# Kernel tuning notes

Measured on AMD Instinct MI355X. Metric: run time of the kernel, lower is better.

The kernel has to match this reference:

```python
import jax, jax.numpy as jnp
import numpy as np
from jax import lax

B, N = 2, 8192
H = W = 256
KNN_K = 33          # includes self, as in _computeDensity
RADIUS = 0.1
CUTOFF = 1.0        # cutOffThreshold: a dx^2 + b dy^2 + c dx dy <= cutoffC
WIN = 9             # fixed splat footprint (ellipse extents ~1-3 px, clamped at 15 in source)
EPS = 1e-8


def setup_inputs() -> dict:
    key = jax.random.key(0)
    k1, k2, k3, k4, k5 = jax.random.split(key, 5)
    points = jax.random.normal(k1, (B, N, 3), jnp.float32)
    # projected pixel coordinates, kept a few px inside the image
    proj_xy = jax.random.uniform(k2, (B, N, 2), jnp.float32, 4.0, W - 4.0)
    # ellipse coefficients a, b, c with 4ab - c^2 > 0 (valid ellipse)
    ab = jax.random.uniform(k3, (B, N, 2), jnp.float32, 0.1, 0.5)
    c = jax.random.uniform(k4, (B, N, 1), jnp.float32, -0.05, 0.05)
    ellipse_params = jnp.concatenate([ab, c], axis=-1)
    colors = jax.random.uniform(k5, (B, N, 3), jnp.float32)
    return {"points": points, "proj_xy": proj_xy,
            "ellipse_params": ellipse_params, "colors": colors}


def _compute_density(points):
    # faithful jax version of _computeDensity: KNN gaussian density
    r2 = RADIUS * RADIUS
    sq = jnp.sum(points * points, axis=-1)                      # [B,N]
    # pairwise squared distances [B,N,N]
    d2 = sq[:, :, None] + sq[:, None, :] - 2.0 * jnp.einsum('bnd,bmd->bnm', points, points)
    neg_d2k, _ = lax.top_k(-d2, KNN_K)                          # k nearest (incl. self)
    d2k = jnp.maximum(-neg_d2k[:, :, 1:], 0.0)                  # drop self, [B,N,K-1]
    w = jnp.exp(-d2k / r2 / 4.0)
    w = jnp.where(d2k > r2, 0.0, w)
    return jnp.sum(w, axis=-1)                                  # [B,N]


def reference(points, proj_xy, ellipse_params, colors):
    density = _compute_density(points)                          # [B,N]
    a = ellipse_params[..., 0]
    b = ellipse_params[..., 1]
    c = ellipse_params[..., 2]
    x = proj_xy[..., 0]
    y = proj_xy[..., 1]
    # _findEllipseBoundingBox extents, clamped at 15 as in the grad path
    den = 4.0 * a * b - c * c
    xE = jnp.minimum(jnp.sqrt(4.0 * b * CUTOFF / den), 15.0)    # [B,N]
    yE = jnp.minimum(jnp.sqrt(4.0 * a * CUTOFF / den), 15.0)

    # fixed WINxWIN footprint around floor(proj) (jit-friendly bbox)
    R = WIN // 2
    offs = jnp.arange(-R, R + 1, dtype=jnp.float32)
    ox, oy = jnp.meshgrid(offs, offs, indexing='ij')
    ox = ox.reshape(-1)                                         # [P]
    oy = oy.reshape(-1)
    x0 = jnp.floor(x)
    y0 = jnp.floor(y)
    px = x0[..., None] + ox                                     # [B,N,P]
    py = y0[..., None] + oy
    dx = px - x[..., None]
    dy = py - y[..., None]
    # elliptical gaussian splat weight, truncated at cutoff
    Q = a[..., None] * dx * dx + b[..., None] * dy * dy + c[..., None] * dx * dy
    inb = (px >= 0) & (px < W) & (py >= 0) & (py < H)
    bbox = (jnp.abs(dx) <= xE[..., None] + 1.0) & (jnp.abs(dy) <= yE[..., None] + 1.0)
    mask = inb & bbox & (Q <= CUTOFF)
    w = jnp.where(mask, jnp.exp(-0.5 * Q) * density[..., None], 0.0)  # [B,N,P]

    # scatter-accumulate weighted colors and weights per pixel
    pxi = jnp.clip(px.astype(jnp.int32), 0, W - 1)
    pyi = jnp.clip(py.astype(jnp.int32), 0, H - 1)
    bi = jnp.arange(B, dtype=jnp.int32)[:, None, None]
    flat = ((bi * H + pyi) * W + pxi).reshape(-1)               # [B*N*P]
    wc = (w[..., None] * colors[:, :, None, :]).reshape(-1, 3)
    wf = w.reshape(-1)
    img_c = jnp.zeros((B * H * W, 3), jnp.float32).at[flat].add(wc)
    img_w = jnp.zeros((B * H * W,), jnp.float32).at[flat].add(wf)
    image = img_c / (img_w[:, None] + EPS)
    return image.reshape(B, H, W, 3)
```

## Files before the change

kernel.cpp:

```cpp
#include <hip/hip_runtime.h>

#define NB  2
#define NP  8192
#define IMH 256
#define IMW 256
#define NBKT 1024
#define CAP 128

constexpr float R2F = 0.01f;
constexpr float BK_SCALE = 64.f;
constexpr float BK_OFF   = 8.f;
#define BK_PAD 7

__device__ __forceinline__ int bucket_of(float x) {
    int b = (int)floorf((x + BK_OFF) * BK_SCALE);
    return min(max(b, 0), NBKT - 1);
}

__device__ __forceinline__ float sq_np(float x, float y, float z) {
    return __fadd_rn(__fadd_rn(__fmul_rn(x, x), __fmul_rn(y, y)),
                     __fmul_rn(z, z));
}

__global__ __launch_bounds__(256) void init_kernel(
    float4* __restrict__ out4, float4* __restrict__ imgw4, int4* __restrict__ cnt4)
{
    const int t = blockIdx.x * 256 + threadIdx.x;
    const float4 z4 = make_float4(0.f, 0.f, 0.f, 0.f);
    if (t < 98304)       out4[t] = z4;
    else if (t < 131072) imgw4[t - 98304] = z4;
    if (t < 512)         cnt4[t] = make_int4(0, 0, 0, 0);
}

__global__ __launch_bounds__(256) void binfill_kernel(
    const float* __restrict__ pts, float4* __restrict__ bins,
    int* __restrict__ counts)
{
    const int t = blockIdx.x * 256 + threadIdx.x;
    const int b = t >> 13, i = t & (NP - 1);
    const float x = pts[(size_t)t * 3 + 0];
    const float y = pts[(size_t)t * 3 + 1];
    const float z = pts[(size_t)t * 3 + 2];
    const int g = (b << 10) + bucket_of(x);
    const int slot = atomicAdd(&counts[g], 1);
    if (slot < CAP)
        bins[(size_t)g * CAP + slot] = make_float4(x, y, z, __int_as_float(i));
}

__global__ __launch_bounds__(1024) void densplat_kernel(
    const float4* __restrict__ bins, const int* __restrict__ counts,
    const float* __restrict__ proj, const float* __restrict__ ell,
    const float* __restrict__ cols,
    float* __restrict__ img_c, float* __restrict__ img_w)
{
    const int bk = blockIdx.x;
    const int b  = bk >> 10, kb = bk & (NBKT - 1);
    const int wave = threadIdx.x >> 6, lane = threadIdx.x & 63;
    const int cnt = min(counts[bk], CAP);
    const int s0  = wave * 8;
    if (s0 >= cnt) return;
    const int nv = min(8, cnt - s0);

    float xi[8], yi[8], zi[8], sqi[8], sum[8];
    int   oi[8];
    #pragma unroll
    for (int u = 0; u < 8; ++u) {
        const int si = s0 + min(u, nv - 1);
        const float4 p = bins[(size_t)bk * CAP + si];
        xi[u] = p.x; yi[u] = p.y; zi[u] = p.z;
        sqi[u] = sq_np(p.x, p.y, p.z);
        oi[u] = __float_as_int(p.w);
        sum[u] = 0.f;
    }

    const int jb0 = max(kb - BK_PAD, 0), jb1 = min(kb + BK_PAD, NBKT - 1);
    for (int jb = jb0; jb <= jb1; ++jb) {
        const int gj = (b << 10) + jb;
        const int cj = min(counts[gj], CAP);
        const float4* __restrict__ bp = bins + (size_t)gj * CAP;
        const bool own = (jb == kb);
        for (int jj = lane; jj < cj; jj += 64) {
            const float4 pj = bp[jj];
            const float sqj = sq_np(pj.x, pj.y, pj.z);
            #pragma unroll
            for (int u = 0; u < 8; ++u) {
                const float dot = __fmaf_rn(zi[u], pj.z,
                                  __fmaf_rn(yi[u], pj.y,
                                  __fmul_rn(xi[u], pj.x)));
                const float d2 = __fsub_rn(__fadd_rn(sqi[u], sqj),
                                           __fadd_rn(dot, dot));
                const float d2c = fmaxf(d2, 0.f);
                if (!(own && jj == s0 + u) && d2c <= R2F)
                    sum[u] += expf(__fmul_rn(__fdiv_rn(d2c, R2F), -0.25f));
            }
        }
    }

    for (int u = 0; u < nv; ++u) {
        float s = sum[u];
        #pragma unroll
        for (int off2 = 32; off2; off2 >>= 1) s += __shfl_down(s, off2, 64);
        const float dens = __shfl(s, 0, 64);
        if (dens == 0.f) continue;

        const size_t gp = (size_t)b * NP + oi[u];
        const float x = proj[gp * 2 + 0], y = proj[gp * 2 + 1];
        const float a  = ell[gp * 3 + 0], bb = ell[gp * 3 + 1], c = ell[gp * 3 + 2];
        const float cr = cols[gp * 3 + 0], cg = cols[gp * 3 + 1], cb = cols[gp * 3 + 2];

        const float den = __fsub_rn(__fmul_rn(__fmul_rn(4.f, a), bb),
                                    __fmul_rn(c, c));
        const float xE = fminf(__fsqrt_rn(__fdiv_rn(__fmul_rn(4.f, bb), den)), 15.f);
        const float yE = fminf(__fsqrt_rn(__fdiv_rn(__fmul_rn(4.f, a),  den)), 15.f);
        const float xEp1 = __fadd_rn(xE, 1.f);
        const float yEp1 = __fadd_rn(yE, 1.f);
        const float x0 = floorf(x), y0 = floorf(y);

        for (int idx = lane; idx < 81; idx += 64) {
            const float ox = (float)(idx / 9) - 4.f;
            const float oy = (float)(idx % 9) - 4.f;
            const float px = __fadd_rn(x0, ox);
            const float py = __fadd_rn(y0, oy);
            if (px < 0.f || px >= 256.f || py < 0.f || py >= 256.f) continue;
            const float dx = __fsub_rn(px, x);
            const float dy = __fsub_rn(py, y);
            if (fabsf(dx) > xEp1 || fabsf(dy) > yEp1) continue;
            const float Q = __fadd_rn(__fadd_rn(
                                __fmul_rn(__fmul_rn(a, dx), dx),
                                __fmul_rn(__fmul_rn(bb, dy), dy)),
                              __fmul_rn(__fmul_rn(c, dx), dy));
            if (!(Q <= 1.0f)) continue;
            const float wgt = __fmul_rn(expf(__fmul_rn(-0.5f, Q)), dens);
            const int pxi = (int)px, pyi = (int)py;
            const int flat = ((b << 8) + pyi) * IMW + pxi;
            atomicAdd(&img_c[flat * 3 + 0], __fmul_rn(wgt, cr));
            atomicAdd(&img_c[flat * 3 + 1], __fmul_rn(wgt, cg));
            atomicAdd(&img_c[flat * 3 + 2], __fmul_rn(wgt, cb));
            atomicAdd(&img_w[flat],         wgt);
        }
    }
}

__global__ __launch_bounds__(256) void norm_kernel(
    float* __restrict__ out, const float* __restrict__ img_w)
{
    const int p = blockIdx.x * 256 + threadIdx.x;
    if (p < NB * IMH * IMW) {
        const float d = __fadd_rn(img_w[p], 1e-8f);
        out[3 * p + 0] = __fdiv_rn(out[3 * p + 0], d);
        out[3 * p + 1] = __fdiv_rn(out[3 * p + 1], d);
        out[3 * p + 2] = __fdiv_rn(out[3 * p + 2], d);
    }
}

extern "C" void kernel_launch(void* const* d_in, const int* in_sizes, int n_in,
                              void* d_out, int out_size, void* d_ws, size_t ws_size,
                              hipStream_t stream)
{
    const float* points = (const float*)d_in[0];
    const float* proj   = (const float*)d_in[1];
    const float* ell    = (const float*)d_in[2];
    const float* cols   = (const float*)d_in[3];
    float* out = (float*)d_out;

    float4* bins   = (float4*)d_ws;
    float*  img_w  = (float*)(bins + (size_t)NB * NBKT * CAP);
    int*    counts = (int*)(img_w + (size_t)NB * IMH * IMW);

    init_kernel    <<<512, 256, 0, stream>>>((float4*)out, (float4*)img_w,
                                             (int4*)counts);
    binfill_kernel <<<NB * NP / 256, 256, 0, stream>>>(points, bins, counts);
    densplat_kernel<<<NB * NBKT, 1024, 0, stream>>>(bins, counts,
                                                    proj, ell, cols, out, img_w);
    norm_kernel    <<<(NB * IMH * IMW + 255) / 256, 256, 0, stream>>>(out, img_w);
}
```

Before: 49.84 us.

## Map one wave per bucket looping over its points, zero buffers with memset

Each bucket used to get a 1024-thread block where each wave handled 8 points. Now each wave owns a whole bucket and loops over its points in groups of 8, with four buckets per 256-thread block. Neighbor bucket counts and pointers are loaded once per wave. The aim is to cut the many mostly idle waves and block launches, since buckets average about 8 points. The image accumulators move to workspace, and the init kernel is replaced by a single hipMemsetAsync over image and count buffers, so norm now reads from img_c. The trade-off is less parallelism for crowded buckets, which are now processed serially within one wave.

```diff
diff --git a/kernel.cpp b/kernel.cpp
--- a/kernel.cpp
+++ b/kernel.cpp
@@ -22,16 +22,6 @@
                      __fmul_rn(z, z));
 }
 
-__global__ __launch_bounds__(256) void init_kernel(
-    float4* __restrict__ out4, float4* __restrict__ imgw4, int4* __restrict__ cnt4)
-{
-    const int t = blockIdx.x * 256 + threadIdx.x;
-    const float4 z4 = make_float4(0.f, 0.f, 0.f, 0.f);
-    if (t < 98304)       out4[t] = z4;
-    else if (t < 131072) imgw4[t - 98304] = z4;
-    if (t < 512)         cnt4[t] = make_int4(0, 0, 0, 0);
-}
-
 __global__ __launch_bounds__(256) void binfill_kernel(
     const float* __restrict__ pts, float4* __restrict__ bins,
     int* __restrict__ counts)
@@ -47,109 +37,120 @@
         bins[(size_t)g * CAP + slot] = make_float4(x, y, z, __int_as_float(i));
 }
 
-__global__ __launch_bounds__(1024) void densplat_kernel(
+__global__ __launch_bounds__(256) void densplat_kernel(
     const float4* __restrict__ bins, const int* __restrict__ counts,
     const float* __restrict__ proj, const float* __restrict__ ell,
     const float* __restrict__ cols,
     float* __restrict__ img_c, float* __restrict__ img_w)
 {
-    const int bk = blockIdx.x;
+    const int wave = threadIdx.x >> 6, lane = threadIdx.x & 63;
+    const int bk = blockIdx.x * 4 + wave;
     const int b  = bk >> 10, kb = bk & (NBKT - 1);
-    const int wave = threadIdx.x >> 6, lane = threadIdx.x & 63;
     const int cnt = min(counts[bk], CAP);
-    const int s0  = wave * 8;
-    if (s0 >= cnt) return;
-    const int nv = min(8, cnt - s0);
-
-    float xi[8], yi[8], zi[8], sqi[8], sum[8];
-    int   oi[8];
-    #pragma unroll
-    for (int u = 0; u < 8; ++u) {
-        const int si = s0 + min(u, nv - 1);
-        const float4 p = bins[(size_t)bk * CAP + si];
-        xi[u] = p.x; yi[u] = p.y; zi[u] = p.z;
-        sqi[u] = sq_np(p.x, p.y, p.z);
-        oi[u] = __float_as_int(p.w);
-        sum[u] = 0.f;
-    }
+    if (cnt == 0) return;
 
     const int jb0 = max(kb - BK_PAD, 0), jb1 = min(kb + BK_PAD, NBKT - 1);
-    for (int jb = jb0; jb <= jb1; ++jb) {
-        const int gj = (b << 10) + jb;
-        const int cj = min(counts[gj], CAP);
-        const float4* __restrict__ bp = bins + (size_t)gj * CAP;
-        const bool own = (jb == kb);
-        for (int jj = lane; jj < cj; jj += 64) {
-            const float4 pj = bp[jj];
-            const float sqj = sq_np(pj.x, pj.y, pj.z);
-            #pragma unroll
-            for (int u = 0; u < 8; ++u) {
-                const float dot = __fmaf_rn(zi[u], pj.z,
-                                  __fmaf_rn(yi[u], pj.y,
-                                  __fmul_rn(xi[u], pj.x)));
-                const float d2 = __fsub_rn(__fadd_rn(sqi[u], sqj),
-                                           __fadd_rn(dot, dot));
-                const float d2c = fmaxf(d2, 0.f);
-                if (!(own && jj == s0 + u) && d2c <= R2F)
-                    sum[u] += expf(__fmul_rn(__fdiv_rn(d2c, R2F), -0.25f));
+    int cj[15]; const float4* bp[15];
+    const int nw = jb1 - jb0 + 1;
+    for (int m = 0; m < nw; ++m) {
+        const int gj = (b << 10) + (jb0 + m);
+        cj[m] = min(counts[gj], CAP);
+        bp[m] = bins + (size_t)gj * CAP;
+    }
+    const int ownm = kb - jb0;
+
+    for (int s0 = 0; s0 < cnt; s0 += 8) {
+        const int nv = min(8, cnt - s0);
+
+        float xi[8], yi[8], zi[8], sqi[8], sum[8];
+        int   oi[8];
+        #pragma unroll
+        for (int u = 0; u < 8; ++u) {
+            const int si = s0 + min(u, nv - 1);
+            const float4 p = bins[(size_t)bk * CAP + si];
+            xi[u] = p.x; yi[u] = p.y; zi[u] = p.z;
+            sqi[u] = sq_np(p.x, p.y, p.z);
+            oi[u] = __float_as_int(p.w);
+            sum[u] = 0.f;
+        }
+
+        for (int m = 0; m < nw; ++m) {
+            const bool own = (m == ownm);
+            const float4* __restrict__ bj = bp[m];
+            const int c = cj[m];
+            for (int jj = lane; jj < c; jj += 64) {
+                const float4 pj = bj[jj];
+                const float sqj = sq_np(pj.x, pj.y, pj.z);
+                #pragma unroll
+                for (int u = 0; u < 8; ++u) {
+                    const float dot = __fmaf_rn(zi[u], pj.z,
+                                      __fmaf_rn(yi[u], pj.y,
+                                      __fmul_rn(xi[u], pj.x)));
+                    const float d2 = __fsub_rn(__fadd_rn(sqi[u], sqj),
+                                               __fadd_rn(dot, dot));
+                    const float d2c = fmaxf(d2, 0.f);
+                    if (!(own && jj == s0 + u) && d2c <= R2F)
+                        sum[u] += expf(__fmul_rn(__fdiv_rn(d2c, R2F), -0.25f));
+                }
             }
         }
-    }
 
-    for (int u = 0; u < nv; ++u) {
-        float s = sum[u];
-        #pragma unroll
-        for (int off2 = 32; off2; off2 >>= 1) s += __shfl_down(s, off2, 64);
-        const float dens = __shfl(s, 0, 64);
-        if (dens == 0.f) continue;
+        for (int u = 0; u < nv; ++u) {
+            float s = sum[u];
+            #pragma unroll
+            for (int off2 = 32; off2; off2 >>= 1) s += __shfl_down(s, off2, 64);
+            const float dens = __shfl(s, 0, 64);
+            if (dens == 0.f) continue;
 
-        const size_t gp = (size_t)b * NP + oi[u];
-        const float x = proj[gp * 2 + 0], y = proj[gp * 2 + 1];
-        const float a  = ell[gp * 3 + 0], bb = ell[gp * 3 + 1], c = ell[gp * 3 + 2];
-        const float cr = cols[gp * 3 + 0], cg = cols[gp * 3 + 1], cb = cols[gp * 3 + 2];
+            const size_t gp = (size_t)b * NP + oi[u];
+            const float x = proj[gp * 2 + 0], y = proj[gp * 2 + 1];
+            const float a  = ell[gp * 3 + 0], bb = ell[gp * 3 + 1], c = ell[gp * 3 + 2];
+            const float cr = cols[gp * 3 + 0], cg = cols[gp * 3 + 1], cb = cols[gp * 3 + 2];
 
-        const float den = __fsub_rn(__fmul_rn(__fmul_rn(4.f, a), bb),
-                                    __fmul_rn(c, c));
-        const float xE = fminf(__fsqrt_rn(__fdiv_rn(__fmul_rn(4.f, bb), den)), 15.f);
-        const float yE = fminf(__fsqrt_rn(__fdiv_rn(__fmul_rn(4.f, a),  den)), 15.f);
-        const float xEp1 = __fadd_rn(xE, 1.f);
-        const float yEp1 = __fadd_rn(yE, 1.f);
-        const float x0 = floorf(x), y0 = floorf(y);
+            const float den = __fsub_rn(__fmul_rn(__fmul_rn(4.f, a), bb),
+                                        __fmul_rn(c, c));
+            const float xE = fminf(__fsqrt_rn(__fdiv_rn(__fmul_rn(4.f, bb), den)), 15.f);
+            const float yE = fminf(__fsqrt_rn(__fdiv_rn(__fmul_rn(4.f, a),  den)), 15.f);
+            const float xEp1 = __fadd_rn(xE, 1.f);
+            const float yEp1 = __fadd_rn(yE, 1.f);
+            const float x0 = floorf(x), y0 = floorf(y);
 
-        for (int idx = lane; idx < 81; idx += 64) {
-            const float ox = (float)(idx / 9) - 4.f;
-            const float oy = (float)(idx % 9) - 4.f;
-            const float px = __fadd_rn(x0, ox);
-            const float py = __fadd_rn(y0, oy);
-            if (px < 0.f || px >= 256.f || py < 0.f || py >= 256.f) continue;
-            const float dx = __fsub_rn(px, x);
-            const float dy = __fsub_rn(py, y);
-            if (fabsf(dx) > xEp1 || fabsf(dy) > yEp1) continue;
-            const float Q = __fadd_rn(__fadd_rn(
-                                __fmul_rn(__fmul_rn(a, dx), dx),
-                                __fmul_rn(__fmul_rn(bb, dy), dy)),
-                              __fmul_rn(__fmul_rn(c, dx), dy));
-            if (!(Q <= 1.0f)) continue;
-            const float wgt = __fmul_rn(expf(__fmul_rn(-0.5f, Q)), dens);
-            const int pxi = (int)px, pyi = (int)py;
-            const int flat = ((b << 8) + pyi) * IMW + pxi;
-            atomicAdd(&img_c[flat * 3 + 0], __fmul_rn(wgt, cr));
-            atomicAdd(&img_c[flat * 3 + 1], __fmul_rn(wgt, cg));
-            atomicAdd(&img_c[flat * 3 + 2], __fmul_rn(wgt, cb));
-            atomicAdd(&img_w[flat],         wgt);
+            for (int idx = lane; idx < 81; idx += 64) {
+                const float ox = (float)(idx / 9) - 4.f;
+                const float oy = (float)(idx % 9) - 4.f;
+                const float px = __fadd_rn(x0, ox);
+                const float py = __fadd_rn(y0, oy);
+                if (px < 0.f || px >= 256.f || py < 0.f || py >= 256.f) continue;
+                const float dx = __fsub_rn(px, x);
+                const float dy = __fsub_rn(py, y);
+                if (fabsf(dx) > xEp1 || fabsf(dy) > yEp1) continue;
+                const float Q = __fadd_rn(__fadd_rn(
+                                    __fmul_rn(__fmul_rn(a, dx), dx),
+                                    __fmul_rn(__fmul_rn(bb, dy), dy)),
+                                  __fmul_rn(__fmul_rn(c, dx), dy));
+                if (!(Q <= 1.0f)) continue;
+                const float wgt = __fmul_rn(expf(__fmul_rn(-0.5f, Q)), dens);
+                const int pxi = (int)px, pyi = (int)py;
+                const int flat = ((b << 8) + pyi) * IMW + pxi;
+                atomicAdd(&img_c[flat * 3 + 0], __fmul_rn(wgt, cr));
+                atomicAdd(&img_c[flat * 3 + 1], __fmul_rn(wgt, cg));
+                atomicAdd(&img_c[flat * 3 + 2], __fmul_rn(wgt, cb));
+                atomicAdd(&img_w[flat],         wgt);
+            }
         }
     }
 }
 
 __global__ __launch_bounds__(256) void norm_kernel(
-    float* __restrict__ out, const float* __restrict__ img_w)
+    float* __restrict__ out, const float* __restrict__ img_c,
+    const float* __restrict__ img_w)
 {
     const int p = blockIdx.x * 256 + threadIdx.x;
     if (p < NB * IMH * IMW) {
         const float d = __fadd_rn(img_w[p], 1e-8f);
-        out[3 * p + 0] = __fdiv_rn(out[3 * p + 0], d);
-        out[3 * p + 1] = __fdiv_rn(out[3 * p + 1], d);
-        out[3 * p + 2] = __fdiv_rn(out[3 * p + 2], d);
+        out[3 * p + 0] = __fdiv_rn(img_c[3 * p + 0], d);
+        out[3 * p + 1] = __fdiv_rn(img_c[3 * p + 1], d);
+        out[3 * p + 2] = __fdiv_rn(img_c[3 * p + 2], d);
     }
 }
 
@@ -164,13 +165,16 @@
     float* out = (float*)d_out;
 
     float4* bins   = (float4*)d_ws;
-    float*  img_w  = (float*)(bins + (size_t)NB * NBKT * CAP);
+    float*  img_c  = (float*)(bins + (size_t)NB * NBKT * CAP);
+    float*  img_w  = img_c + (size_t)NB * IMH * IMW * 3;
     int*    counts = (int*)(img_w + (size_t)NB * IMH * IMW);
+    const size_t zero_bytes = sizeof(float) * ((size_t)NB * IMH * IMW * 4)
+                            + sizeof(int) * (NB * NBKT);
 
-    init_kernel    <<<512, 256, 0, stream>>>((float4*)out, (float4*)img_w,
-                                             (int4*)counts);
+    hipMemsetAsync(img_c, 0, zero_bytes, stream);
     binfill_kernel <<<NB * NP / 256, 256, 0, stream>>>(points, bins, counts);
-    densplat_kernel<<<NB * NBKT, 1024, 0, stream>>>(bins, counts,
-                                                    proj, ell, cols, out, img_w);
-    norm_kernel    <<<(NB * IMH * IMW + 255) / 256, 256, 0, stream>>>(out, img_w);
+    densplat_kernel<<<NB * NBKT / 4, 256, 0, stream>>>(bins, counts,
+                                                       proj, ell, cols,
+                                                       img_c, img_w);
+    norm_kernel    <<<(NB * IMH * IMW + 255) / 256, 256, 0, stream>>>(out, img_c, img_w);
 }
```

Result: slower. 193.9 us (+289.1%).
